# Kernel optimization log

Measured on AMD Instinct MI355X. Metric: run time of the kernel, lower is better.

## Reference

```python
import jax, jax.numpy as jnp
import numpy as np

SEQ_LEN = 2048
NUM_GLOBAL = 32
NEG_INF = float('-inf')


def _build_mask(seq_len=SEQ_LEN, num_global=NUM_GLOBAL):
    # Causal mask: triu(ones).T == lower-triangular ones; zeros -> -inf, ones -> 0.
    m = np.where(np.tril(np.ones((seq_len, seq_len), dtype=np.float32)) == 1.0, 0.0, NEG_INF)
    # Deterministic 'random.sample' of global tokens (fixed for reproducibility).
    rng = np.random.default_rng(0)
    gtok = rng.choice(seq_len, size=num_global, replace=False)
    m[:, gtok] = 0.0
    m[gtok, :] = 0.0
    return jnp.asarray(m)


def setup_inputs() -> dict:
    key = jax.random.key(0)
    ks = jax.random.split(key, 9)
    B, S, D_IN, D_QK = 8, SEQ_LEN, 1024, 128
    return {
        'q': jax.random.normal(ks[0], (B, S, D_IN), dtype=jnp.float32),
        'k': jax.random.normal(ks[1], (B, S, D_IN), dtype=jnp.float32),
        'v': jax.random.normal(ks[2], (B, S, D_IN), dtype=jnp.float32),
        'Wq': jax.random.normal(ks[3], (D_QK, D_IN), dtype=jnp.float32) * 0.02,
        'bq': jax.random.normal(ks[4], (D_QK,), dtype=jnp.float32) * 0.02,
        'Wk': jax.random.normal(ks[5], (D_QK, D_IN), dtype=jnp.float32) * 0.02,
        'bk': jax.random.normal(ks[6], (D_QK,), dtype=jnp.float32) * 0.02,
        'Wv': jax.random.normal(ks[7], (D_QK, D_IN), dtype=jnp.float32) * 0.02,
        'bv': jax.random.normal(ks[8], (D_QK,), dtype=jnp.float32) * 0.02,
    }


def reference(q, k, v, Wq, bq, Wk, bk, Wv, bv):
    # Linear projections (torch nn.Linear: x @ W.T + b)
    Q = jnp.einsum('bsd,qd->bsq', q, Wq) + bq   # [B,S,dq]
    K = jnp.einsum('bsd,qd->bsq', k, Wk) + bk   # [B,S,dk]
    V = jnp.einsum('bsd,qd->bsq', v, Wv) + bv   # [B,S,dk]
    mask = _build_mask()                        # [S,S] static causal+global
    scale = K.shape[-1] ** 0.5
    scores = jnp.einsum('bqd,bkd->bqk', Q, K)   # dense QK^T [B,S,S]
    scores = (scores + mask) / scale            # (-inf stays -inf)
    attn = jax.nn.softmax(scores, axis=-1)
    return jnp.einsum('bqk,bkd->bqd', attn, V)
```

## Files before the change

### kernel.cpp

```cpp
#include <hip/hip_runtime.h>
#include <cstdint>

constexpr int SEQ  = 2048;
constexpr int DIN  = 1024;
constexpr int DQK  = 128;
constexpr int NB   = 8;
constexpr int MTOT = NB * SEQ;
constexpr float INV_SCALE = 0.08838834764831845f;

typedef __attribute__((ext_vector_type(8))) short  short8;
typedef __attribute__((ext_vector_type(4))) float  floatx4;
typedef __attribute__((ext_vector_type(4))) int    intx4;

struct GM { unsigned long long w[32]; };

static void compute_gtok(unsigned long long bits[32]) {
  typedef unsigned __int128 u128;
  uint32_t pool[4];
  uint32_t hc = 0x43b0d7e5u;
  auto hashmix = [&hc](uint32_t v) -> uint32_t {
    v ^= hc; hc *= 0x931e8875u; v *= hc; v ^= v >> 16; return v;
  };
  auto mixf = [](uint32_t x, uint32_t y) -> uint32_t {
    uint32_t r = x * 0xca01f9ddu - y * 0x4973f715u;
    r ^= r >> 16; return r;
  };
  pool[0] = hashmix(0u);
  for (int i = 1; i < 4; ++i) pool[i] = hashmix(0u);
  for (int s = 0; s < 4; ++s)
    for (int d = 0; d < 4; ++d)
      if (s != d) pool[d] = mixf(pool[d], hashmix(pool[s]));
  uint32_t hb = 0x8b51f9ddu;
  uint32_t st[8];
  for (int i = 0; i < 8; ++i) {
    uint32_t dv = pool[i & 3];
    dv ^= hb; hb *= 0x58f38dedu; dv *= hb; dv ^= dv >> 16;
    st[i] = dv;
  }
  uint64_t sv[4];
  for (int i = 0; i < 4; ++i)
    sv[i] = (uint64_t)st[2 * i] | ((uint64_t)st[2 * i + 1] << 32);
  const u128 MUL = ((u128)2549297995355413924ULL << 64) | (u128)4865540595714422341ULL;
  u128 initstate = ((u128)sv[0] << 64) | sv[1];
  u128 initseq   = ((u128)sv[2] << 64) | sv[3];
  u128 state = 0;
  u128 inc = (initseq << 1) | 1;
  state = state * MUL + inc;
  state += initstate;
  state = state * MUL + inc;
  bool has32 = false; uint32_t cache32 = 0;
  auto next64 = [&]() -> uint64_t {
    state = state * MUL + inc;
    uint64_t hi = (uint64_t)(state >> 64);
    uint64_t lo = (uint64_t)state;
    unsigned rot = (unsigned)(state >> 122);
    uint64_t x = hi ^ lo;
    return (x >> rot) | (x << ((64u - rot) & 63u));
  };
  auto next32 = [&]() -> uint32_t {
    if (has32) { has32 = false; return cache32; }
    uint64_t n = next64();
    has32 = true; cache32 = (uint32_t)(n >> 32);
    return (uint32_t)n;
  };
  bool in_set[SEQ];
  for (int i = 0; i < SEQ; ++i) in_set[i] = false;
  for (uint32_t j = 2016; j < 2048; ++j) {
    uint32_t rng_excl = j + 1;
    uint64_t m = (uint64_t)next32() * rng_excl;
    uint32_t leftover = (uint32_t)m;
    if (leftover < rng_excl) {
      uint32_t threshold = (0xFFFFFFFFu - j) % rng_excl;
      while (leftover < threshold) {
        m = (uint64_t)next32() * rng_excl;
        leftover = (uint32_t)m;
      }
    }
    uint32_t val = (uint32_t)(m >> 32);
    if (in_set[val]) in_set[j] = true;
    else in_set[val] = true;
  }
  for (int i = 0; i < 32; ++i) bits[i] = 0ULL;
  for (int t = 0; t < SEQ; ++t)
    if (in_set[t]) bits[t >> 6] |= (1ULL << (t & 63));
}

__device__ __forceinline__ float bf2f(unsigned short h) {
  return __uint_as_float(((unsigned)h) << 16);
}
__device__ __forceinline__ void ldsld16(const void* g, void* l) {
  __builtin_amdgcn_global_load_lds(
      (const __attribute__((address_space(1))) unsigned int*)g,
      (__attribute__((address_space(3))) unsigned int*)l, 16, 0, 0);
}
__device__ __forceinline__ bool gbit(const GM& g, int j) {
  return (g.w[j >> 6] >> (j & 63)) & 1ULL;
}
__device__ __forceinline__ void split4(float4 x, unsigned hw[2], unsigned lw[2]) {
  unsigned u0 = __float_as_uint(x.x), u1 = __float_as_uint(x.y);
  unsigned u2 = __float_as_uint(x.z), u3 = __float_as_uint(x.w);
  hw[0] = __builtin_amdgcn_perm(u1, u0, 0x07060302u);
  hw[1] = __builtin_amdgcn_perm(u3, u2, 0x07060302u);
  unsigned r0 = __float_as_uint(x.x - __uint_as_float(u0 & 0xFFFF0000u));
  unsigned r1 = __float_as_uint(x.y - __uint_as_float(u1 & 0xFFFF0000u));
  unsigned r2 = __float_as_uint(x.z - __uint_as_float(u2 & 0xFFFF0000u));
  unsigned r3 = __float_as_uint(x.w - __uint_as_float(u3 & 0xFFFF0000u));
  lw[0] = __builtin_amdgcn_perm(r1, r0, 0x07060302u);
  lw[1] = __builtin_amdgcn_perm(r3, r2, 0x07060302u);
}
__device__ __forceinline__ void split1(float v, unsigned short& h, unsigned short& l) {
  unsigned u = __float_as_uint(v);
  h = (unsigned short)(u >> 16);
  float rr = v - __uint_as_float(u & 0xFFFF0000u);
  l = (unsigned short)(__float_as_uint(rr) >> 16);
}

__global__ __launch_bounds__(256) void wconv_kernel(
    const float* __restrict__ Wq, const float* __restrict__ Wk, const float* __restrict__ Wv,
    unsigned short* __restrict__ Whi, unsigned short* __restrict__ Wlo) {
  const float* W = blockIdx.y == 0 ? Wq : blockIdx.y == 1 ? Wk : Wv;
  size_t base = (size_t)blockIdx.y * DQK * DIN;
  int e = (blockIdx.x * 256 + threadIdx.x) * 4;
  float4 x = *(const float4*)&W[e];
  unsigned hw[2], lw[2];
  split4(x, hw, lw);
  *(uint2*)&Whi[base + e] = make_uint2(hw[0], hw[1]);
  *(uint2*)&Wlo[base + e] = make_uint2(lw[0], lw[1]);
}

__global__ __launch_bounds__(256, 2) void proj_kernel(
    const float* __restrict__ xq, const float* __restrict__ xk, const float* __restrict__ xv,
    const unsigned short* __restrict__ Whi, const unsigned short* __restrict__ Wlo,
    const float* __restrict__ bq, const float* __restrict__ bk, const float* __restrict__ bv,
    unsigned short* __restrict__ Qb, unsigned short* __restrict__ Kb,
    unsigned short* __restrict__ Vth, unsigned short* __restrict__ Vtl) {
  const int which = blockIdx.y;
  const float* X    = which == 0 ? xq : which == 1 ? xk : xv;
  const float* bias = which == 0 ? bq : which == 1 ? bk : bv;
  const int m0 = blockIdx.x * 128;

  __shared__ unsigned short sm[4][8192];

  const int tid = threadIdx.x;
  const int w = tid >> 6, lane = tid & 63, l15 = lane & 15, quad = lane >> 4;
  const int mh = (w >> 1) * 64, nh = (w & 1) * 64;

  floatx4 acc[4][4] = {};
  float biasv[4];
#pragma unroll
  for (int j = 0; j < 4; ++j) biasv[j] = bias[nh + j * 16 + l15];

  const unsigned short* WhiP = Whi + (size_t)which * DQK * DIN;
  const unsigned short* WloP = Wlo + (size_t)which * DQK * DIN;

  for (int kb = 0; kb < DIN; kb += 64) {
    __syncthreads();
#pragma unroll
    for (int i = 0; i < 8; ++i) {
      int f = tid + i * 256;
      int r = f >> 4, c4 = f & 15;
      float4 x = *(const float4*)&X[(size_t)(m0 + r) * DIN + kb + c4 * 4];
      unsigned hw[2], lw[2];
      split4(x, hw, lw);
      int off = r * 64 + (((c4 >> 1) ^ (r & 7)) * 8) + (c4 & 1) * 4;
      *(uint2*)&sm[0][off] = make_uint2(hw[0], hw[1]);
      *(uint2*)&sm[1][off] = make_uint2(lw[0], lw[1]);
    }
#pragma unroll
    for (int i = 0; i < 8; ++i) {
      int c = w * 8 + i;
      int plane = c >> 4, cc = c & 15;
      int F = cc * 1024 + lane * 16;
      int n = F >> 7, gs = (F >> 4) & 7, gl = gs ^ (n & 7);
      const unsigned short* gp = (plane ? WloP : WhiP) + (size_t)n * DIN + kb + gl * 8;
      ldsld16(gp, (char*)&sm[2 + plane][0] + cc * 1024);
    }
    __syncthreads();
#pragma unroll
    for (int ks = 0; ks < 2; ++ks) {
      short8 Ah[4], Al[4], Bh[4], Bl[4];
#pragma unroll
      for (int ms = 0; ms < 4; ++ms) {
        int off = (mh + ms * 16 + l15) * 64 + (((ks * 4 + quad) ^ (l15 & 7)) * 8);
        Ah[ms] = *(const short8*)&sm[0][off];
        Al[ms] = *(const short8*)&sm[1][off];
      }
#pragma unroll
      for (int ns = 0; ns < 4; ++ns) {
        int off = (nh + ns * 16 + l15) * 64 + (((ks * 4 + quad) ^ (l15 & 7)) * 8);
        Bh[ns] = *(const short8*)&sm[2][off];
        Bl[ns] = *(const short8*)&sm[3][off];
      }
#pragma unroll
      for (int i = 0; i < 4; ++i)
#pragma unroll
        for (int j = 0; j < 4; ++j) {
          floatx4 c = acc[i][j];
          c = __builtin_amdgcn_mfma_f32_16x16x32_bf16(Ah[i], Bh[j], c, 0, 0, 0);
          c = __builtin_amdgcn_mfma_f32_16x16x32_bf16(Ah[i], Bl[j], c, 0, 0, 0);
          c = __builtin_amdgcn_mfma_f32_16x16x32_bf16(Al[i], Bh[j], c, 0, 0, 0);
          acc[i][j] = c;
        }
    }
  }

  if (which < 2) {
    unsigned short* O = which == 0 ? Qb : Kb;
#pragma unroll
    for (int i = 0; i < 4; ++i)
#pragma unroll
      for (int j = 0; j < 4; ++j)
#pragma unroll
        for (int r = 0; r < 4; ++r) {
          int m = mh + i * 16 + quad * 4 + r;
          int n = nh + j * 16 + l15;
          float v = acc[i][j][r] + biasv[j];
          O[(size_t)(m0 + m) * DQK + n] =
              (unsigned short)((__float_as_uint(v) + 0x7FFFu +
                                ((__float_as_uint(v) >> 16) & 1u)) >> 16);
        }
  } else {
    __syncthreads();
    unsigned short* VH = &sm[0][0];
    unsigned short* VL = &sm[2][0];
#pragma unroll
    for (int i = 0; i < 4; ++i)
#pragma unroll
      for (int j = 0; j < 4; ++j)
#pragma unroll
        for (int r = 0; r < 4; ++r) {
          int s = mh + i * 16 + quad * 4 + r;
          int d = nh + j * 16 + l15;
          float v = acc[i][j][r] + biasv[j];
          unsigned short h, lo;
          split1(v, h, lo);
          int off = d * 128 + (((s >> 3) ^ (d & 15)) * 8) + (s & 7);
          VH[off] = h; VL[off] = lo;
        }
    __syncthreads();
    int b = m0 >> 11, s0 = m0 & 2047;
#pragma unroll
    for (int i = 0; i < 8; ++i) {
      int cch = i * 256 + tid;
      int d = cch >> 4, gI = cch & 15;
      int loff = d * 128 + ((gI ^ (d & 15)) * 8);
      intx4 vh = *(const intx4*)&VH[loff];
      intx4 vl = *(const intx4*)&VL[loff];
      size_t go = ((size_t)b * DQK + d) * SEQ + s0 + gI * 8;
      *(intx4*)&Vth[go] = vh;
      *(intx4*)&Vtl[go] = vl;
    }
  }
}

__global__ __launch_bounds__(256, 2) void attn_kernel(
    const unsigned short* __restrict__ Qb, const unsigned short* __restrict__ Kb,
    const unsigned short* __restrict__ Vth, const unsigned short* __restrict__ Vtl,
    float* __restrict__ Opart, float2* __restrict__ ML, GM g, unsigned int t64) {
  __shared__ unsigned short Ks[64 * 128];
  __shared__ unsigned short Vh[128 * 64];
  __shared__ unsigned short Vl[128 * 64];
  __shared__ unsigned short Ph[4][16 * 80];
  __shared__ unsigned short Pl[4][16 * 80];

  const int tid = threadIdx.x;
  const int w = tid >> 6, lane = tid & 63, l15 = lane & 15, quad = lane >> 4;
  const int b = blockIdx.y;
  const int qt = blockIdx.x >> 1, half = blockIdx.x & 1;
  const int qs = qt * 64;

  short8 qf[4];
  const unsigned short* Qrow = Qb + ((size_t)(b * SEQ + qs + w * 16 + l15)) * DQK;
#pragma unroll
  for (int j = 0; j < 4; ++j) qf[j] = *(const short8*)&Qrow[j * 32 + quad * 8];

  int rowi[4]; bool growb[4];
#pragma unroll
  for (int r = 0; r < 4; ++r) {
    rowi[r] = qs + w * 16 + quad * 4 + r;
    growb[r] = gbit(g, rowi[r]);
  }

  floatx4 o[8] = {};
  float m_r[4] = {-1e30f, -1e30f, -1e30f, -1e30f};
  float l_r[4] = {0.f, 0.f, 0.f, 0.f};

  const bool qhasg = (t64 >> qt) & 1;
  const unsigned short* KbB = Kb  + (size_t)b * SEQ * DQK;
  const unsigned short* VhB = Vth + (size_t)b * DQK * SEQ;
  const unsigned short* VlB = Vtl + (size_t)b * DQK * SEQ;

  for (int kt = half; kt < 32; kt += 2) {
    const int ks0 = kt * 64;
    if (!((ks0 <= qs + 63) || ((t64 >> kt) & 1) || qhasg)) continue;

    __syncthreads();
#pragma unroll
    for (int i = 0; i < 12; ++i) {
      int c = w * 12 + i;
      if (c < 16) {
        int F = c * 1024 + lane * 16;
        int r = F >> 8, gs = (F >> 4) & 15, gl = gs ^ (r & 15);
        ldsld16(KbB + (size_t)(ks0 + r) * DQK + gl * 8, (char*)Ks + c * 1024);
      } else if (c < 32) {
        int cc = c - 16;
        int F = cc * 1024 + lane * 16;
        int d = F >> 7, gs = (F >> 4) & 7, gl = gs ^ (d & 7);
        ldsld16(VhB + (size_t)d * SEQ + ks0 + gl * 8, (char*)Vh + cc * 1024);
      } else {
        int cc = c - 32;
        int F = cc * 1024 + lane * 16;
        int d = F >> 7, gs = (F >> 4) & 7, gl = gs ^ (d & 7);
        ldsld16(VlB + (size_t)d * SEQ + ks0 + gl * 8, (char*)Vl + cc * 1024);
      }
    }
    __syncthreads();

    floatx4 S[4];
#pragma unroll
    for (int c4 = 0; c4 < 4; ++c4) {
      floatx4 s = {0.f, 0.f, 0.f, 0.f};
#pragma unroll
      for (int j = 0; j < 4; ++j) {
        short8 kf = *(const short8*)&Ks[(c4 * 16 + l15) * 128 + (((j * 4 + quad) ^ l15) * 8)];
        s = __builtin_amdgcn_mfma_f32_16x16x32_bf16(qf[j], kf, s, 0, 0, 0);
      }
      S[c4] = s;
    }

    float z[4][4];
    float mx[4] = {-1e30f, -1e30f, -1e30f, -1e30f};
#pragma unroll
    for (int c4 = 0; c4 < 4; ++c4) {
      int col = ks0 + c4 * 16 + l15;
      bool cg = gbit(g, col);
#pragma unroll
      for (int r = 0; r < 4; ++r) {
        bool ok = (col <= rowi[r]) || cg || growb[r];
        float zz = ok ? S[c4][r] * INV_SCALE : -1e30f;
        z[c4][r] = zz;
        mx[r] = fmaxf(mx[r], zz);
      }
    }
#pragma unroll
    for (int d = 1; d < 16; d <<= 1)
#pragma unroll
      for (int r = 0; r < 4; ++r) mx[r] = fmaxf(mx[r], __shfl_xor(mx[r], d));
    float alpha[4], rs[4] = {0.f, 0.f, 0.f, 0.f};
#pragma unroll
    for (int r = 0; r < 4; ++r) {
      float mn = fmaxf(m_r[r], mx[r]);
      alpha[r] = __expf(m_r[r] - mn);
      m_r[r] = mn;
    }
    float p[4][4];
#pragma unroll
    for (int c4 = 0; c4 < 4; ++c4)
#pragma unroll
      for (int r = 0; r < 4; ++r) {
        float pp = __expf(z[c4][r] - m_r[r]);
        p[c4][r] = pp;
        rs[r] += pp;
      }
#pragma unroll
    for (int d = 1; d < 16; d <<= 1)
#pragma unroll
      for (int r = 0; r < 4; ++r) rs[r] += __shfl_xor(rs[r], d);
#pragma unroll
    for (int r = 0; r < 4; ++r) l_r[r] = l_r[r] * alpha[r] + rs[r];
#pragma unroll
    for (int n = 0; n < 8; ++n)
#pragma unroll
      for (int r = 0; r < 4; ++r) o[n][r] *= alpha[r];

#pragma unroll
    for (int c4 = 0; c4 < 4; ++c4)
#pragma unroll
      for (int r = 0; r < 4; ++r) {
        unsigned short h, lo;
        split1(p[c4][r], h, lo);
        int off = (quad * 4 + r) * 80 + c4 * 16 + l15;
        Ph[w][off] = h; Pl[w][off] = lo;
      }
    short8 pf[2], pg[2];
#pragma unroll
    for (int kq = 0; kq < 2; ++kq) {
      int off = l15 * 80 + kq * 32 + quad * 8;
      pf[kq] = *(const short8*)&Ph[w][off];
      pg[kq] = *(const short8*)&Pl[w][off];
    }

#pragma unroll
    for (int n = 0; n < 8; ++n) {
      int drow = n * 16 + l15;
#pragma unroll
      for (int kq = 0; kq < 2; ++kq) {
        int off = drow * 64 + (((kq * 4 + quad) ^ (drow & 7)) * 8);
        short8 vhf = *(const short8*)&Vh[off];
        short8 vlf = *(const short8*)&Vl[off];
        floatx4 c = o[n];
        c = __builtin_amdgcn_mfma_f32_16x16x32_bf16(pf[kq], vhf, c, 0, 0, 0);
        c = __builtin_amdgcn_mfma_f32_16x16x32_bf16(pg[kq], vhf, c, 0, 0, 0);
        c = __builtin_amdgcn_mfma_f32_16x16x32_bf16(pf[kq], vlf, c, 0, 0, 0);
        o[n] = c;
      }
    }
  }

  const size_t grp = (size_t)(b * 32 + qt) * 2 + half;
  float* Op = Opart + grp * 64 * 128;
#pragma unroll
  for (int n = 0; n < 8; ++n)
#pragma unroll
    for (int r = 0; r < 4; ++r)
      Op[(w * 16 + quad * 4 + r) * 128 + n * 16 + l15] = o[n][r];
  if (l15 == 0) {
#pragma unroll
    for (int r = 0; r < 4; ++r)
      ML[grp * 64 + w * 16 + quad * 4 + r] = make_float2(m_r[r], l_r[r]);
  }
}

__global__ __launch_bounds__(256) void merge_kernel(
    const float* __restrict__ Opart, const float2* __restrict__ ML,
    float* __restrict__ Out) {
  const int t = threadIdx.x;
  const int row = blockIdx.x * 2 + (t >> 7);
  const int col = t & 127;
  const int grp = row >> 6;
  const int rin = row & 63;
  const size_t i0 = ((size_t)grp * 2 + 0) * 64 + rin;
  const size_t i1 = ((size_t)grp * 2 + 1) * 64 + rin;
  const float2 ml0 = ML[i0], ml1 = ML[i1];
  const float m = fmaxf(ml0.x, ml1.x);
  const float w0 = __expf(ml0.x - m), w1 = __expf(ml1.x - m);
  const float denom = w0 * ml0.y + w1 * ml1.y;
  const float o0 = Opart[i0 * 128 + col], o1 = Opart[i1 * 128 + col];
  Out[(size_t)row * 128 + col] = (w0 * o0 + w1 * o1) / denom;
}

extern "C" void kernel_launch(void* const* d_in, const int* in_sizes, int n_in,
                              void* d_out, int out_size, void* d_ws, size_t ws_size,
                              hipStream_t stream) {
  const float* q  = (const float*)d_in[0];
  const float* k  = (const float*)d_in[1];
  const float* v  = (const float*)d_in[2];
  const float* Wq = (const float*)d_in[3];
  const float* bq = (const float*)d_in[4];
  const float* Wk = (const float*)d_in[5];
  const float* bk = (const float*)d_in[6];
  const float* Wv = (const float*)d_in[7];
  const float* bv = (const float*)d_in[8];
  float* out = (float*)d_out;

  unsigned short* Qb  = (unsigned short*)d_ws;
  unsigned short* Kb2 = Qb  + (size_t)MTOT * DQK;
  unsigned short* Vth = Kb2 + (size_t)MTOT * DQK;
  unsigned short* Vtl = Vth + (size_t)MTOT * DQK;
  unsigned short* Whi = Vtl + (size_t)MTOT * DQK;
  unsigned short* Wlo = Whi + (size_t)3 * DQK * DIN;
  float*  Opart = (float*)(Wlo + (size_t)3 * DQK * DIN);
  float2* ML    = (float2*)(Opart + (size_t)2 * MTOT * DQK);

  GM g;
  compute_gtok(g.w);
  unsigned int t64 = 0;
  for (int t = 0; t < 32; ++t) if (g.w[t] != 0ULL) t64 |= (1u << t);

  hipLaunchKernelGGL(wconv_kernel, dim3(128, 3), dim3(256), 0, stream,
                     Wq, Wk, Wv, Whi, Wlo);
  hipLaunchKernelGGL(proj_kernel, dim3(128, 3), dim3(256), 0, stream,
                     q, k, v, Whi, Wlo, bq, bk, bv, Qb, Kb2, Vth, Vtl);
  hipLaunchKernelGGL(attn_kernel, dim3(64, 8), dim3(256), 0, stream,
                     Qb, Kb2, Vth, Vtl, Opart, ML, g, t64);
  hipLaunchKernelGGL(merge_kernel, dim3(MTOT / 2), dim3(256), 0, stream,
                     Opart, ML, out);
}
```

Before: 293.5 us.

## Drop V low-part split, shrink projection tiles, split attention KV across three blocks

Stores V as a single rounded bf16 plane instead of a hi/lo pair, which removes the Vtl buffer, its LDS staging, and one MFMA per PV step. The projection kernel now uses 64-row tiles with twice as many blocks and a higher occupancy bound. The attention kernel splits the key range three ways instead of two, and the merge kernel combines three partials. The cost is lower precision for V and more partial-output traffic in the merge.

```diff
diff --git a/kernel.cpp b/kernel.cpp
--- a/kernel.cpp
+++ b/kernel.cpp
@@ -85,9 +85,6 @@
     if (in_set[t]) bits[t >> 6] |= (1ULL << (t & 63));
 }
 
-__device__ __forceinline__ float bf2f(unsigned short h) {
-  return __uint_as_float(((unsigned)h) << 16);
-}
 __device__ __forceinline__ void ldsld16(const void* g, void* l) {
   __builtin_amdgcn_global_load_lds(
       (const __attribute__((address_space(1))) unsigned int*)g,
@@ -114,6 +111,10 @@
   float rr = v - __uint_as_float(u & 0xFFFF0000u);
   l = (unsigned short)(__float_as_uint(rr) >> 16);
 }
+__device__ __forceinline__ unsigned short bfr_rne(float v) {
+  unsigned u = __float_as_uint(v);
+  return (unsigned short)((u + 0x7FFFu + ((u >> 16) & 1u)) >> 16);
+}
 
 __global__ __launch_bounds__(256) void wconv_kernel(
     const float* __restrict__ Wq, const float* __restrict__ Wk, const float* __restrict__ Wv,
@@ -128,24 +129,27 @@
   *(uint2*)&Wlo[base + e] = make_uint2(lw[0], lw[1]);
 }
 
-__global__ __launch_bounds__(256, 2) void proj_kernel(
+__global__ __launch_bounds__(256, 3) void proj_kernel(
     const float* __restrict__ xq, const float* __restrict__ xk, const float* __restrict__ xv,
     const unsigned short* __restrict__ Whi, const unsigned short* __restrict__ Wlo,
     const float* __restrict__ bq, const float* __restrict__ bk, const float* __restrict__ bv,
     unsigned short* __restrict__ Qb, unsigned short* __restrict__ Kb,
-    unsigned short* __restrict__ Vth, unsigned short* __restrict__ Vtl) {
+    unsigned short* __restrict__ Vth) {
   const int which = blockIdx.y;
   const float* X    = which == 0 ? xq : which == 1 ? xk : xv;
   const float* bias = which == 0 ? bq : which == 1 ? bk : bv;
-  const int m0 = blockIdx.x * 128;
-
-  __shared__ unsigned short sm[4][8192];
+  const int m0 = blockIdx.x * 64;
+
+  __shared__ unsigned short Xh[64 * 64];
+  __shared__ unsigned short Xl[64 * 64];
+  __shared__ unsigned short Wh[128 * 64];
+  __shared__ unsigned short Wl[128 * 64];
 
   const int tid = threadIdx.x;
   const int w = tid >> 6, lane = tid & 63, l15 = lane & 15, quad = lane >> 4;
-  const int mh = (w >> 1) * 64, nh = (w & 1) * 64;
-
-  floatx4 acc[4][4] = {};
+  const int mh = (w >> 1) * 32, nh = (w & 1) * 64;
+
+  floatx4 acc[2][4] = {};
   float biasv[4];
 #pragma unroll
   for (int j = 0; j < 4; ++j) biasv[j] = bias[nh + j * 16 + l15];
@@ -156,15 +160,15 @@
   for (int kb = 0; kb < DIN; kb += 64) {
     __syncthreads();
 #pragma unroll
-    for (int i = 0; i < 8; ++i) {
+    for (int i = 0; i < 4; ++i) {
       int f = tid + i * 256;
       int r = f >> 4, c4 = f & 15;
       float4 x = *(const float4*)&X[(size_t)(m0 + r) * DIN + kb + c4 * 4];
       unsigned hw[2], lw[2];
       split4(x, hw, lw);
       int off = r * 64 + (((c4 >> 1) ^ (r & 7)) * 8) + (c4 & 1) * 4;
-      *(uint2*)&sm[0][off] = make_uint2(hw[0], hw[1]);
-      *(uint2*)&sm[1][off] = make_uint2(lw[0], lw[1]);
+      *(uint2*)&Xh[off] = make_uint2(hw[0], hw[1]);
+      *(uint2*)&Xl[off] = make_uint2(lw[0], lw[1]);
     }
 #pragma unroll
     for (int i = 0; i < 8; ++i) {
@@ -173,26 +177,26 @@
       int F = cc * 1024 + lane * 16;
       int n = F >> 7, gs = (F >> 4) & 7, gl = gs ^ (n & 7);
       const unsigned short* gp = (plane ? WloP : WhiP) + (size_t)n * DIN + kb + gl * 8;
-      ldsld16(gp, (char*)&sm[2 + plane][0] + cc * 1024);
+      ldsld16(gp, (char*)(plane ? Wl : Wh) + cc * 1024);
     }
     __syncthreads();
 #pragma unroll
     for (int ks = 0; ks < 2; ++ks) {
-      short8 Ah[4], Al[4], Bh[4], Bl[4];
-#pragma unroll
-      for (int ms = 0; ms < 4; ++ms) {
+      short8 Ah[2], Al[2], Bh[4], Bl[4];
+#pragma unroll
+      for (int ms = 0; ms < 2; ++ms) {
         int off = (mh + ms * 16 + l15) * 64 + (((ks * 4 + quad) ^ (l15 & 7)) * 8);
-        Ah[ms] = *(const short8*)&sm[0][off];
-        Al[ms] = *(const short8*)&sm[1][off];
+        Ah[ms] = *(const short8*)&Xh[off];
+        Al[ms] = *(const short8*)&Xl[off];
       }
 #pragma unroll
       for (int ns = 0; ns < 4; ++ns) {
         int off = (nh + ns * 16 + l15) * 64 + (((ks * 4 + quad) ^ (l15 & 7)) * 8);
-        Bh[ns] = *(const short8*)&sm[2][off];
-        Bl[ns] = *(const short8*)&sm[3][off];
-      }
-#pragma unroll
-      for (int i = 0; i < 4; ++i)
+        Bh[ns] = *(const short8*)&Wh[off];
+        Bl[ns] = *(const short8*)&Wl[off];
+      }
+#pragma unroll
+      for (int i = 0; i < 2; ++i)
 #pragma unroll
         for (int j = 0; j < 4; ++j) {
           floatx4 c = acc[i][j];
@@ -207,66 +211,55 @@
   if (which < 2) {
     unsigned short* O = which == 0 ? Qb : Kb;
 #pragma unroll
-    for (int i = 0; i < 4; ++i)
+    for (int i = 0; i < 2; ++i)
 #pragma unroll
       for (int j = 0; j < 4; ++j)
 #pragma unroll
         for (int r = 0; r < 4; ++r) {
           int m = mh + i * 16 + quad * 4 + r;
           int n = nh + j * 16 + l15;
-          float v = acc[i][j][r] + biasv[j];
-          O[(size_t)(m0 + m) * DQK + n] =
-              (unsigned short)((__float_as_uint(v) + 0x7FFFu +
-                                ((__float_as_uint(v) >> 16) & 1u)) >> 16);
+          O[(size_t)(m0 + m) * DQK + n] = bfr_rne(acc[i][j][r] + biasv[j]);
         }
   } else {
     __syncthreads();
-    unsigned short* VH = &sm[0][0];
-    unsigned short* VL = &sm[2][0];
-#pragma unroll
-    for (int i = 0; i < 4; ++i)
+    unsigned short* VH = Wh;
+#pragma unroll
+    for (int i = 0; i < 2; ++i)
 #pragma unroll
       for (int j = 0; j < 4; ++j)
 #pragma unroll
         for (int r = 0; r < 4; ++r) {
           int s = mh + i * 16 + quad * 4 + r;
           int d = nh + j * 16 + l15;
-          float v = acc[i][j][r] + biasv[j];
-          unsigned short h, lo;
-          split1(v, h, lo);
-          int off = d * 128 + (((s >> 3) ^ (d & 15)) * 8) + (s & 7);
-          VH[off] = h; VL[off] = lo;
+          VH[d * 64 + (((s >> 3) ^ (d & 7)) * 8) + (s & 7)] =
+              bfr_rne(acc[i][j][r] + biasv[j]);
         }
     __syncthreads();
     int b = m0 >> 11, s0 = m0 & 2047;
 #pragma unroll
-    for (int i = 0; i < 8; ++i) {
+    for (int i = 0; i < 4; ++i) {
       int cch = i * 256 + tid;
-      int d = cch >> 4, gI = cch & 15;
-      int loff = d * 128 + ((gI ^ (d & 15)) * 8);
+      int d = cch >> 3, gI = cch & 7;
+      int loff = d * 64 + ((gI ^ (d & 7)) * 8);
       intx4 vh = *(const intx4*)&VH[loff];
-      intx4 vl = *(const intx4*)&VL[loff];
-      size_t go = ((size_t)b * DQK + d) * SEQ + s0 + gI * 8;
-      *(intx4*)&Vth[go] = vh;
-      *(intx4*)&Vtl[go] = vl;
-    }
-  }
-}
-
-__global__ __launch_bounds__(256, 2) void attn_kernel(
+      *(intx4*)&Vth[((size_t)b * DQK + d) * SEQ + s0 + gI * 8] = vh;
+    }
+  }
+}
+
+__global__ __launch_bounds__(256, 3) void attn_kernel(
     const unsigned short* __restrict__ Qb, const unsigned short* __restrict__ Kb,
-    const unsigned short* __restrict__ Vth, const unsigned short* __restrict__ Vtl,
+    const unsigned short* __restrict__ Vth,
     float* __restrict__ Opart, float2* __restrict__ ML, GM g, unsigned int t64) {
   __shared__ unsigned short Ks[64 * 128];
   __shared__ unsigned short Vh[128 * 64];
-  __shared__ unsigned short Vl[128 * 64];
-  __shared__ unsigned short Ph[4][16 * 80];
-  __shared__ unsigned short Pl[4][16 * 80];
+  __shared__ unsigned short Ph[4][16 * 72];
+  __shared__ unsigned short Pl[4][16 * 72];
 
   const int tid = threadIdx.x;
   const int w = tid >> 6, lane = tid & 63, l15 = lane & 15, quad = lane >> 4;
   const int b = blockIdx.y;
-  const int qt = blockIdx.x >> 1, half = blockIdx.x & 1;
+  const int qt = blockIdx.x / 3, s3 = blockIdx.x - qt * 3;
   const int qs = qt * 64;
 
   short8 qf[4];
@@ -288,30 +281,24 @@
   const bool qhasg = (t64 >> qt) & 1;
   const unsigned short* KbB = Kb  + (size_t)b * SEQ * DQK;
   const unsigned short* VhB = Vth + (size_t)b * DQK * SEQ;
-  const unsigned short* VlB = Vtl + (size_t)b * DQK * SEQ;
-
-  for (int kt = half; kt < 32; kt += 2) {
+
+  for (int kt = s3; kt < 32; kt += 3) {
     const int ks0 = kt * 64;
     if (!((ks0 <= qs + 63) || ((t64 >> kt) & 1) || qhasg)) continue;
 
     __syncthreads();
 #pragma unroll
-    for (int i = 0; i < 12; ++i) {
-      int c = w * 12 + i;
+    for (int i = 0; i < 8; ++i) {
+      int c = w * 8 + i;
       if (c < 16) {
         int F = c * 1024 + lane * 16;
         int r = F >> 8, gs = (F >> 4) & 15, gl = gs ^ (r & 15);
         ldsld16(KbB + (size_t)(ks0 + r) * DQK + gl * 8, (char*)Ks + c * 1024);
-      } else if (c < 32) {
+      } else {
         int cc = c - 16;
         int F = cc * 1024 + lane * 16;
         int d = F >> 7, gs = (F >> 4) & 7, gl = gs ^ (d & 7);
         ldsld16(VhB + (size_t)d * SEQ + ks0 + gl * 8, (char*)Vh + cc * 1024);
-      } else {
-        int cc = c - 32;
-        int F = cc * 1024 + lane * 16;
-        int d = F >> 7, gs = (F >> 4) & 7, gl = gs ^ (d & 7);
-        ldsld16(VlB + (size_t)d * SEQ + ks0 + gl * 8, (char*)Vl + cc * 1024);
       }
     }
     __syncthreads();
@@ -379,13 +366,13 @@
       for (int r = 0; r < 4; ++r) {
         unsigned short h, lo;
         split1(p[c4][r], h, lo);
-        int off = (quad * 4 + r) * 80 + c4 * 16 + l15;
+        int off = (quad * 4 + r) * 72 + c4 * 16 + l15;
         Ph[w][off] = h; Pl[w][off] = lo;
       }
     short8 pf[2], pg[2];
 #pragma unroll
     for (int kq = 0; kq < 2; ++kq) {
-      int off = l15 * 80 + kq * 32 + quad * 8;
+      int off = l15 * 72 + kq * 32 + quad * 8;
       pf[kq] = *(const short8*)&Ph[w][off];
       pg[kq] = *(const short8*)&Pl[w][off];
     }
@@ -397,17 +384,15 @@
       for (int kq = 0; kq < 2; ++kq) {
         int off = drow * 64 + (((kq * 4 + quad) ^ (drow & 7)) * 8);
         short8 vhf = *(const short8*)&Vh[off];
-        short8 vlf = *(const short8*)&Vl[off];
         floatx4 c = o[n];
         c = __builtin_amdgcn_mfma_f32_16x16x32_bf16(pf[kq], vhf, c, 0, 0, 0);
         c = __builtin_amdgcn_mfma_f32_16x16x32_bf16(pg[kq], vhf, c, 0, 0, 0);
-        c = __builtin_amdgcn_mfma_f32_16x16x32_bf16(pf[kq], vlf, c, 0, 0, 0);
         o[n] = c;
       }
     }
   }
 
-  const size_t grp = (size_t)(b * 32 + qt) * 2 + half;
+  const size_t grp = (size_t)(b * 32 + qt) * 3 + s3;
   float* Op = Opart + grp * 64 * 128;
 #pragma unroll
   for (int n = 0; n < 8; ++n)
@@ -429,14 +414,17 @@
   const int col = t & 127;
   const int grp = row >> 6;
   const int rin = row & 63;
-  const size_t i0 = ((size_t)grp * 2 + 0) * 64 + rin;
-  const size_t i1 = ((size_t)grp * 2 + 1) * 64 + rin;
-  const float2 ml0 = ML[i0], ml1 = ML[i1];
-  const float m = fmaxf(ml0.x, ml1.x);
-  const float w0 = __expf(ml0.x - m), w1 = __expf(ml1.x - m);
-  const float denom = w0 * ml0.y + w1 * ml1.y;
-  const float o0 = Opart[i0 * 128 + col], o1 = Opart[i1 * 128 + col];
-  Out[(size_t)row * 128 + col] = (w0 * o0 + w1 * o1) / denom;
+  const size_t base = (size_t)grp * 3;
+  float2 ml0 = ML[(base + 0) * 64 + rin];
+  float2 ml1 = ML[(base + 1) * 64 + rin];
+  float2 ml2 = ML[(base + 2) * 64 + rin];
+  const float m = fmaxf(fmaxf(ml0.x, ml1.x), ml2.x);
+  const float w0 = __expf(ml0.x - m), w1 = __expf(ml1.x - m), w2 = __expf(ml2.x - m);
+  const float denom = w0 * ml0.y + w1 * ml1.y + w2 * ml2.y;
+  const float o0 = Opart[((base + 0) * 64 + rin) * 128 + col];
+  const float o1 = Opart[((base + 1) * 64 + rin) * 128 + col];
+  const float o2 = Opart[((base + 2) * 64 + rin) * 128 + col];
+  Out[(size_t)row * 128 + col] = (w0 * o0 + w1 * o1 + w2 * o2) / denom;
 }
 
 extern "C" void kernel_launch(void* const* d_in, const int* in_sizes, int n_in,
@@ -456,11 +444,10 @@
   unsigned short* Qb  = (unsigned short*)d_ws;
   unsigned short* Kb2 = Qb  + (size_t)MTOT * DQK;
   unsigned short* Vth = Kb2 + (size_t)MTOT * DQK;
-  unsigned short* Vtl = Vth + (size_t)MTOT * DQK;
-  unsigned short* Whi = Vtl + (size_t)MTOT * DQK;
+  unsigned short* Whi = Vth + (size_t)MTOT * DQK;
   unsigned short* Wlo = Whi + (size_t)3 * DQK * DIN;
   float*  Opart = (float*)(Wlo + (size_t)3 * DQK * DIN);
-  float2* ML    = (float2*)(Opart + (size_t)2 * MTOT * DQK);
+  float2* ML    = (float2*)(Opart + (size_t)3 * MTOT * DQK);
 
   GM g;
   compute_gtok(g.w);
@@ -469,10 +456,10 @@
 
   hipLaunchKernelGGL(wconv_kernel, dim3(128, 3), dim3(256), 0, stream,
                      Wq, Wk, Wv, Whi, Wlo);
-  hipLaunchKernelGGL(proj_kernel, dim3(128, 3), dim3(256), 0, stream,
-                     q, k, v, Whi, Wlo, bq, bk, bv, Qb, Kb2, Vth, Vtl);
-  hipLaunchKernelGGL(attn_kernel, dim3(64, 8), dim3(256), 0, stream,
-                     Qb, Kb2, Vth, Vtl, Opart, ML, g, t64);
+  hipLaunchKernelGGL(proj_kernel, dim3(256, 3), dim3(256), 0, stream,
+                     q, k, v, Whi, Wlo, bq, bk, bv, Qb, Kb2, Vth);
+  hipLaunchKernelGGL(attn_kernel, dim3(96, 8), dim3(256), 0, stream,
+                     Qb, Kb2, Vth, Opart, ML, g, t64);
   hipLaunchKernelGGL(merge_kernel, dim3(MTOT / 2), dim3(256), 0, stream,
                      Opart, ML, out);
 }
```

Result: faster. 280.0 us (-4.6%).
